# Performance work log

Measured on AMD Instinct MI355X. Metric: run time of the kernel, lower is better.

Reference implementation:

```python
import jax, jax.numpy as jnp
import numpy as np

D_MODEL = 768
NUM_HEADS = 12
D_K = D_MODEL // NUM_HEADS
B, T = 2, 4096


def setup_inputs() -> dict:
    key = jax.random.key(0)
    ks = jax.random.split(key, 5)
    x = jax.random.normal(ks[0], (B, T, D_MODEL), dtype=jnp.float32)
    # causal mask: True = masked (matches masked_fill semantics)
    mask = jnp.triu(jnp.ones((T, T), dtype=bool), k=1)
    W_qkv = jax.random.normal(ks[1], (D_MODEL, 3 * D_MODEL), dtype=jnp.float32) / np.sqrt(D_MODEL)
    b_qkv = jax.random.normal(ks[2], (3 * D_MODEL,), dtype=jnp.float32) * 0.02
    W_out = jax.random.normal(ks[3], (D_MODEL, D_MODEL), dtype=jnp.float32) / np.sqrt(D_MODEL)
    b_out = jax.random.normal(ks[4], (D_MODEL,), dtype=jnp.float32) * 0.02
    return {"x": x, "mask": mask, "W_qkv": W_qkv, "b_qkv": b_qkv, "W_out": W_out, "b_out": b_out}


def reference(x, mask, W_qkv, b_qkv, W_out, b_out):
    Bb, Tt, C = x.shape
    qkv = x @ W_qkv + b_qkv                       # [B,T,3C]
    # torch: reshape(B,T,H,3*d_k).transpose(1,2) then chunk on last dim
    qkv = qkv.reshape(Bb, Tt, NUM_HEADS, 3, D_K)  # split each head's 3*d_k chunk
    qkv = jnp.transpose(qkv, (0, 2, 1, 3, 4))     # [B,H,T,3,d_k]
    q, k, v = qkv[..., 0, :], qkv[..., 1, :], qkv[..., 2, :]
    scores = jnp.einsum('bhqd,bhkd->bhqk', q, k) / np.sqrt(D_K)
    scores = jnp.where(mask[None, None], -jnp.inf, scores)
    attn = jax.nn.softmax(scores, axis=-1)
    context = jnp.einsum('bhqk,bhkd->bhqd', attn, v)
    context = jnp.transpose(context, (0, 2, 1, 3)).reshape(Bb, Tt, C)
    return context @ W_out + b_out
```

## Files before the change

kernel.cpp:

```cpp
#include <hip/hip_runtime.h>
#include <hip/hip_bf16.h>
#include <stdint.h>


typedef __attribute__((ext_vector_type(8))) short bf16x8;
typedef __attribute__((ext_vector_type(4))) short bf16x4;
typedef __attribute__((ext_vector_type(4))) float f32x4;

#define TT 4096
#define NH 12
#define DK 64
#define DMODEL 768
#define NQKV 2304

__device__ __forceinline__ unsigned short f2bf(float f) {
    union { float f; unsigned u; } v; v.f = f;
    unsigned u = v.u;
    return (unsigned short)((u + 0x7fffu + ((u >> 16) & 1u)) >> 16);
}
__device__ __forceinline__ unsigned fbits(float f) {
    union { float f; unsigned u; } v; v.f = f; return v.u;
}
__device__ __forceinline__ unsigned pack_bf2(float a, float b) {
    return __builtin_amdgcn_perm(fbits(b) + 0x8000u, fbits(a) + 0x8000u, 0x07060302u);
}
__device__ __forceinline__ void glds16(const void* g, void* l) {
    __builtin_amdgcn_global_load_lds(
        (const __attribute__((address_space(1))) void*)g,
        (__attribute__((address_space(3))) void*)l, 16, 0, 0);
}

__global__ __launch_bounds__(256)
void prep(const float* __restrict__ x, unsigned short* __restrict__ xb,
          const float* __restrict__ Wq, unsigned short* __restrict__ Wqt,
          const float* __restrict__ Wo, unsigned short* __restrict__ Wot) {
    int b = blockIdx.x;
    if (b < 6144) {
        int i = (b * 256 + threadIdx.x) * 4;
        float4 v = *(const float4*)(x + i);
        uint2 u;
        u.x = pack_bf2(v.x, v.y);
        u.y = pack_bf2(v.z, v.w);
        *(uint2*)(xb + i) = u;
        return;
    }
    __shared__ unsigned short tile[64][65];
    const float* W; unsigned short* Wt; int K, N, bx, by;
    if (b < 6144 + 432) {
        int bb = b - 6144; bx = bb % 36; by = bb / 36;
        W = Wq; Wt = Wqt; K = DMODEL; N = NQKV;
    } else {
        int bb = b - 6576; bx = bb % 12; by = bb / 12;
        W = Wo; Wt = Wot; K = DMODEL; N = DMODEL;
    }
    int k0 = by * 64, n0 = bx * 64;
    int c = threadIdx.x & 63;
    int r0 = threadIdx.x >> 6;
    for (int p = 0; p < 16; ++p) {
        int r = r0 + p * 4;
        tile[r][c] = f2bf(W[(size_t)(k0 + r) * N + n0 + c]);
    }
    __syncthreads();
    for (int p = 0; p < 16; ++p) {
        int n = r0 + p * 4;
        Wt[(size_t)(n0 + n) * K + k0 + c] = tile[c][n];
    }
}

__global__ __launch_bounds__(256, 4)
void gemm_qkv(const unsigned short* __restrict__ Amat, const unsigned short* __restrict__ Bmat,
              const float* __restrict__ bias, unsigned short* __restrict__ qb,
              unsigned short* __restrict__ kb, unsigned short* __restrict__ vtb) {
    __shared__ unsigned short As[128 * 64];
    __shared__ unsigned short Bs[128 * 64];
    const int K = DMODEL;
    int bid = (int)blockIdx.y * 64 + (int)blockIdx.x;
    int idx = bid >> 3;
    int n0 = ((bid & 7) * 8 + (idx & 7)) * 128;
    int m0 = (idx >> 3) * 128;
    int tid = threadIdx.x, lane = tid & 63, w = tid >> 6;
    int wm = (w >> 1) * 64, wn = (w & 1) * 64;
    int quad = lane >> 4, lc = lane & 15;

    int gc8 = ((lane & 7) ^ (lane >> 3)) * 8;
    int row0 = w * 32 + (lane >> 3);
    const unsigned short* agp0 = Amat + (size_t)(m0 + row0) * K + gc8;
    const unsigned short* bgp0 = Bmat + (size_t)(n0 + row0) * K + gc8;
    unsigned short* alp0 = &As[w * 4 * 512];
    unsigned short* blp0 = &Bs[w * 4 * 512];

    int foff[2];
    for (int h = 0; h < 2; ++h)
        foff[h] = lc * 64 + (((quad + 4 * h) ^ (lc & 7)) * 8);

    f32x4 acc[4][4];
    for (int a = 0; a < 4; ++a)
        for (int b2 = 0; b2 < 4; ++b2) acc[a][b2] = (f32x4){0.f, 0.f, 0.f, 0.f};

    for (int k0 = 0; k0 < K; k0 += 64) {
        {
            const unsigned short* ag = agp0;
            const unsigned short* bg = bgp0;
            for (int p = 0; p < 4; ++p) {
                glds16(ag, alp0 + p * 512);
                glds16(bg, blp0 + p * 512);
                ag += 8 * DMODEL; bg += 8 * DMODEL;
            }
            agp0 += 64; bgp0 += 64;
        }
        __syncthreads();
        bf16x8 bfr[4][2];
        for (int nt = 0; nt < 4; ++nt)
            for (int h = 0; h < 2; ++h)
                bfr[nt][h] = *(const bf16x8*)(&Bs[wn * 64 + nt * 1024 + foff[h]]);
        for (int mt = 0; mt < 4; ++mt) {
            bf16x8 af0 = *(const bf16x8*)(&As[wm * 64 + mt * 1024 + foff[0]]);
            bf16x8 af1 = *(const bf16x8*)(&As[wm * 64 + mt * 1024 + foff[1]]);
            for (int nt = 0; nt < 4; ++nt) {
                acc[mt][nt] = __builtin_amdgcn_mfma_f32_16x16x32_bf16(
                    af0, bfr[nt][0], acc[mt][nt], 0, 0, 0);
                acc[mt][nt] = __builtin_amdgcn_mfma_f32_16x16x32_bf16(
                    af1, bfr[nt][1], acc[mt][nt], 0, 0, 0);
            }
        }
        __syncthreads();
    }
    const float c2q = 0.18033688f;
    for (int mt = 0; mt < 4; ++mt) {
        int colv = m0 + wm + mt * 16 + quad * 4;
        float4 bv = *(const float4*)(bias + colv);
        int h = colv / 192;
        int r = colv - h * 192;
        int which = r >> 6;
        int d0 = r & 63;
        for (int nt = 0; nt < 4; ++nt) {
            int tok = n0 + wn + nt * 16 + lc;
            int b = tok >> 12, t = tok & 4095;
            size_t bh = (size_t)(b * NH + h);
            float v0 = acc[mt][nt][0] + bv.x, v1 = acc[mt][nt][1] + bv.y;
            float v2 = acc[mt][nt][2] + bv.z, v3 = acc[mt][nt][3] + bv.w;
            if (which == 0) {
                uint2 u;
                u.x = pack_bf2(v0 * c2q, v1 * c2q);
                u.y = pack_bf2(v2 * c2q, v3 * c2q);
                *(uint2*)(qb + (bh * TT + t) * DK + d0) = u;
            } else if (which == 1) {
                uint2 u;
                u.x = pack_bf2(v0, v1);
                u.y = pack_bf2(v2, v3);
                *(uint2*)(kb + (bh * TT + t) * DK + d0) = u;
            } else {
                unsigned short* vp = vtb + (bh * DK + d0) * TT + t;
                vp[0] = f2bf(v0); vp[TT] = f2bf(v1);
                vp[2 * TT] = f2bf(v2); vp[3 * TT] = f2bf(v3);
            }
        }
    }
}

template <bool DIAG>
__device__ __forceinline__ void flash_tile(const unsigned short* __restrict__ Kb,
                                           const unsigned short* __restrict__ Vb,
                                           bf16x8 qf0, bf16x8 qf1,
                                           f32x4 (&o)[4], f32x4& ol,
                                           int kt, int q_lo, int quad, int lc) {
    int c0 = quad ^ (lc & 7);
    int sw = lc & 7;
    const bf16x4 ones = {(short)0x3F80, (short)0x3F80, (short)0x3F80, (short)0x3F80};
    for (int ktile = 0; ktile < 4; ++ktile) {
        bf16x8 kf0 = *(const bf16x8*)(&Kb[(ktile * 16 + lc) * 64 + c0 * 8]);
        bf16x8 kf1 = *(const bf16x8*)(&Kb[(ktile * 16 + lc) * 64 + (c0 ^ 4) * 8]);
        f32x4 s = (f32x4){0.f, 0.f, 0.f, 0.f};
        __builtin_amdgcn_s_setprio(1);
        s = __builtin_amdgcn_mfma_f32_16x16x32_bf16(kf0, qf0, s, 0, 0, 0);
        s = __builtin_amdgcn_mfma_f32_16x16x32_bf16(kf1, qf1, s, 0, 0, 0);
        __builtin_amdgcn_s_setprio(0);
        float p[4];
        if (DIAG) {
            int key0 = kt + ktile * 16 + quad * 4;
            int qcol = q_lo + lc;
            for (int i = 0; i < 4; ++i) {
                float e = __builtin_amdgcn_exp2f(s[i]);
                if (key0 + i > qcol) e = 0.f;
                p[i] = e;
            }
        } else {
            for (int i = 0; i < 4; ++i) p[i] = __builtin_amdgcn_exp2f(s[i]);
        }
        union { uint2 u; bf16x4 v; } pc;
        pc.u.x = pack_bf2(p[0], p[1]);
        pc.u.y = pack_bf2(p[2], p[3]);
        int c8 = (ktile * 2 + (quad >> 1)) ^ sw;
        int voff = c8 * 8 + (quad & 1) * 4;
        __builtin_amdgcn_s_setprio(1);
        ol = __builtin_amdgcn_mfma_f32_16x16x16bf16_1k(ones, pc.v, ol, 0, 0, 0);
        for (int dt = 0; dt < 4; ++dt) {
            bf16x4 vf = *(const bf16x4*)(&Vb[(dt * 16 + lc) * 64 + voff]);
            o[dt] = __builtin_amdgcn_mfma_f32_16x16x16bf16_1k(vf, pc.v, o[dt], 0, 0, 0);
        }
        __builtin_amdgcn_s_setprio(0);
    }
}

__global__ __launch_bounds__(256)
void flash_attn(const unsigned short* __restrict__ qbuf,
                const unsigned short* __restrict__ kbuf,
                const unsigned short* __restrict__ vtbuf,
                unsigned short* __restrict__ ctx) {
    __shared__ unsigned short Ks[2][64 * 64];
    __shared__ unsigned short Vs[2][64 * 64];
    int bh = blockIdx.x;
    int qblk = 63 - (int)blockIdx.y;
    int tid = threadIdx.x, lane = tid & 63, w = tid >> 6;
    int quad = lane >> 4, lc = lane & 15;
    const size_t base = (size_t)bh * TT * DK;
    int col8 = ((lane & 7) ^ (lane >> 3)) * 8;
    size_t hb = (size_t)(bh / NH) * TT * DMODEL + (size_t)(bh % NH) * DK;

    int q_lo = qblk * 64 + w * 16;
    int ntile = qblk + 1;

    int rb = (w & 1) * 4;
    const unsigned short* sgp[4];
    int stepEls;
    if (w < 2) {
        const unsigned short* kb0 = kbuf + base + (size_t)(lane >> 3) * DK + col8;
        for (int r = 0; r < 4; ++r) sgp[r] = kb0 + (size_t)((rb + r) * 8) * DK;
        stepEls = 64 * DK;
    } else {
        const unsigned short* vb0 = vtbuf + base + (size_t)(lane >> 3) * TT + col8;
        for (int r = 0; r < 4; ++r) sgp[r] = vb0 + (size_t)((rb + r) * 8) * TT;
        stepEls = 64;
    }

    bf16x8 qf0, qf1;
    {
        const unsigned short* qp = qbuf + base + (size_t)(q_lo + lc) * DK;
        qf0 = *(const bf16x8*)(qp + quad * 8);
        qf1 = *(const bf16x8*)(qp + 32 + quad * 8);
    }
    f32x4 o[4];
    for (int dt = 0; dt < 4; ++dt) o[dt] = (f32x4){0.f, 0.f, 0.f, 0.f};
    f32x4 ol = (f32x4){0.f, 0.f, 0.f, 0.f};

    {
        if (w < 2)
            for (int r = 0; r < 4; ++r) {
                glds16(sgp[r], &Ks[0][(rb + r) * 512]);
                sgp[r] += stepEls;
            }
        else
            for (int r = 0; r < 4; ++r) {
                glds16(sgp[r], &Vs[0][(rb + r) * 512]);
                sgp[r] += stepEls;
            }
    }
    __syncthreads();

    for (int ti = 0; ti < ntile; ++ti) {
        int cur = ti & 1;
        if (ti + 1 < ntile) {
            if (w < 2)
                for (int r = 0; r < 4; ++r) {
                    glds16(sgp[r], &Ks[cur ^ 1][(rb + r) * 512]);
                    sgp[r] += stepEls;
                }
            else
                for (int r = 0; r < 4; ++r) {
                    glds16(sgp[r], &Vs[cur ^ 1][(rb + r) * 512]);
                    sgp[r] += stepEls;
                }
        }
        int kt = ti * 64;
        if (ti == ntile - 1)
            flash_tile<true>(&Ks[cur][0], &Vs[cur][0], qf0, qf1, o, ol,
                             kt, q_lo, quad, lc);
        else
            flash_tile<false>(&Ks[cur][0], &Vs[cur][0], qf0, qf1, o, ol,
                              kt, q_lo, quad, lc);
        __syncthreads();
    }

    float inv = 1.f / ol[0];
    int t = q_lo + lc;
    unsigned short* cp = ctx + hb + (size_t)t * DMODEL;
    for (int dt = 0; dt < 4; ++dt) {
        uint2 u;
        u.x = pack_bf2(o[dt][0] * inv, o[dt][1] * inv);
        u.y = pack_bf2(o[dt][2] * inv, o[dt][3] * inv);
        *(uint2*)(cp + dt * 16 + quad * 4) = u;
    }
}

__global__ __launch_bounds__(256, 4)
void gemm_out(const unsigned short* __restrict__ Amat, const unsigned short* __restrict__ Bmat,
              const float* __restrict__ bias, float* __restrict__ out) {
    __shared__ unsigned short S[(64 + 128) * 64];
    const int K = DMODEL;
    int bid = (int)blockIdx.y * 64 + (int)blockIdx.x;
    int idx = bid >> 3;
    int n0 = ((bid & 7) * 8 + (idx & 7)) * 128;
    int m0 = (idx >> 3) * 64;
    int tid = threadIdx.x, lane = tid & 63, w = tid >> 6;
    int wm = (w & 1) * 32, wn = (w >> 1) * 64;
    int quad = lane >> 4, lc = lane & 15;

    const unsigned short* gp[6]; unsigned short* lp[6];
    for (int p = 0; p < 6; ++p) {
        int c = (w * 6 + p) * 64 + lane;
        if (c < 512) {
            int row = c >> 3, gc = (c & 7) ^ (row & 7);
            gp[p] = Amat + (size_t)(m0 + row) * K + gc * 8;
        } else {
            int cb = c - 512;
            int row = cb >> 3, gc = (cb & 7) ^ (row & 7);
            gp[p] = Bmat + (size_t)(n0 + row) * K + gc * 8;
        }
        lp[p] = &S[(w * 6 + p) * 512];
    }
    int foffA[2][2], foffB[4][2];
    for (int mt = 0; mt < 2; ++mt)
        for (int h = 0; h < 2; ++h)
            foffA[mt][h] = (wm + mt * 16 + lc) * 64 + (((quad + 4 * h) ^ (lc & 7)) * 8);
    for (int nt = 0; nt < 4; ++nt)
        for (int h = 0; h < 2; ++h)
            foffB[nt][h] = 4096 + (wn + nt * 16 + lc) * 64 + (((quad + 4 * h) ^ (lc & 7)) * 8);

    f32x4 acc[2][4];
    for (int a = 0; a < 2; ++a)
        for (int b2 = 0; b2 < 4; ++b2) acc[a][b2] = (f32x4){0.f, 0.f, 0.f, 0.f};

    for (int k0 = 0; k0 < K; k0 += 64) {
        for (int p = 0; p < 6; ++p) {
            glds16(gp[p], lp[p]);
            gp[p] += 64;
        }
        __syncthreads();
        bf16x8 af[2][2], bfr[4][2];
        for (int mt = 0; mt < 2; ++mt)
            for (int h = 0; h < 2; ++h) af[mt][h] = *(const bf16x8*)(&S[foffA[mt][h]]);
        for (int nt = 0; nt < 4; ++nt)
            for (int h = 0; h < 2; ++h) bfr[nt][h] = *(const bf16x8*)(&S[foffB[nt][h]]);
        for (int mt = 0; mt < 2; ++mt)
            for (int nt = 0; nt < 4; ++nt) {
                acc[mt][nt] = __builtin_amdgcn_mfma_f32_16x16x32_bf16(
                    af[mt][0], bfr[nt][0], acc[mt][nt], 0, 0, 0);
                acc[mt][nt] = __builtin_amdgcn_mfma_f32_16x16x32_bf16(
                    af[mt][1], bfr[nt][1], acc[mt][nt], 0, 0, 0);
            }
        __syncthreads();
    }
    for (int mt = 0; mt < 2; ++mt) {
        int colv = m0 + wm + mt * 16 + quad * 4;
        float4 bv = *(const float4*)(bias + colv);
        for (int nt = 0; nt < 4; ++nt) {
            int tok = n0 + wn + nt * 16 + lc;
            float4 ov;
            ov.x = acc[mt][nt][0] + bv.x;
            ov.y = acc[mt][nt][1] + bv.y;
            ov.z = acc[mt][nt][2] + bv.z;
            ov.w = acc[mt][nt][3] + bv.w;
            *(float4*)(out + (size_t)tok * DMODEL + colv) = ov;
        }
    }
}

extern "C" void kernel_launch(void* const* d_in, const int* in_sizes, int n_in,
                              void* d_out, int out_size, void* d_ws, size_t ws_size,
                              hipStream_t stream) {
    const float* x     = (const float*)d_in[0];
    const float* W_qkv = (const float*)d_in[2];
    const float* b_qkv = (const float*)d_in[3];
    const float* W_out = (const float*)d_in[4];
    const float* b_out = (const float*)d_in[5];
    float* out = (float*)d_out;

    unsigned short* ws = (unsigned short*)d_ws;
    unsigned short* Wqkv_t = ws;
    unsigned short* Wout_t = Wqkv_t + (size_t)NQKV * DMODEL;
    unsigned short* q_buf  = Wout_t + (size_t)DMODEL * DMODEL;
    unsigned short* k_buf  = q_buf  + (size_t)2 * NH * TT * DK;
    unsigned short* vt_buf = k_buf  + (size_t)2 * NH * TT * DK;
    unsigned short* ctx    = vt_buf + (size_t)2 * NH * TT * DK;
    unsigned short* x_bf   = ctx;

    prep<<<dim3(6720), 256, 0, stream>>>(x, x_bf, W_qkv, Wqkv_t, W_out, Wout_t);
    gemm_qkv<<<dim3((2 * TT) / 128, NQKV / 128), 256, 0, stream>>>(
        Wqkv_t, x_bf, b_qkv, q_buf, k_buf, vt_buf);
    flash_attn<<<dim3(2 * NH, TT / 64), 256, 0, stream>>>(q_buf, k_buf, vt_buf, ctx);
    gemm_out<<<dim3((2 * TT) / 128, DMODEL / 64), 256, 0, stream>>>(
        Wout_t, ctx, b_out, out);
}
```

Measured before the change: 254.8 us.

## Enlarge QKV GEMM M-tile to 192 and use hardware bf16 pack conversion

The QKV projection GEMM tile grows from 128x128 to 192x128 along the weight dimension, so each block does 6x4 MFMA sub-tiles per wave and the grid drops from 18 to 12 rows. Occupancy is lowered to 3 blocks per CU to make room for the larger accumulator set. Separately, the manual round-and-permute bf16 packing in the QKV epilogue, the attention P conversion and the context store is replaced with the native v_cvt_pk_bf16_f32 instruction. This cuts instruction count in the attention inner loop and raises operand reuse in the GEMM, at the cost of higher register pressure and fewer resident waves.

New measurement: 255.3 us (median of 2 runs). Within noise of the previous version (+0.2%).

```diff
diff --git a/kernel.cpp b/kernel.cpp
--- a/kernel.cpp
+++ b/kernel.cpp
@@ -23,6 +23,11 @@
 }
 __device__ __forceinline__ unsigned pack_bf2(float a, float b) {
     return __builtin_amdgcn_perm(fbits(b) + 0x8000u, fbits(a) + 0x8000u, 0x07060302u);
+}
+__device__ __forceinline__ unsigned cvt_pk_bf16(float a, float b) {
+    unsigned r;
+    asm("v_cvt_pk_bf16_f32 %0, %1, %2" : "=v"(r) : "v"(a), "v"(b));
+    return r;
 }
 __device__ __forceinline__ void glds16(const void* g, void* l) {
     __builtin_amdgcn_global_load_lds(
@@ -67,44 +72,48 @@
     }
 }
 
-__global__ __launch_bounds__(256, 4)
+__global__ __launch_bounds__(256, 3)
 void gemm_qkv(const unsigned short* __restrict__ Amat, const unsigned short* __restrict__ Bmat,
               const float* __restrict__ bias, unsigned short* __restrict__ qb,
               unsigned short* __restrict__ kb, unsigned short* __restrict__ vtb) {
-    __shared__ unsigned short As[128 * 64];
+    __shared__ unsigned short As[192 * 64];
     __shared__ unsigned short Bs[128 * 64];
     const int K = DMODEL;
     int bid = (int)blockIdx.y * 64 + (int)blockIdx.x;
     int idx = bid >> 3;
     int n0 = ((bid & 7) * 8 + (idx & 7)) * 128;
-    int m0 = (idx >> 3) * 128;
+    int m0 = (idx >> 3) * 192;
     int tid = threadIdx.x, lane = tid & 63, w = tid >> 6;
-    int wm = (w >> 1) * 64, wn = (w & 1) * 64;
+    int wm = (w >> 1) * 96, wn = (w & 1) * 64;
     int quad = lane >> 4, lc = lane & 15;
 
     int gc8 = ((lane & 7) ^ (lane >> 3)) * 8;
-    int row0 = w * 32 + (lane >> 3);
-    const unsigned short* agp0 = Amat + (size_t)(m0 + row0) * K + gc8;
-    const unsigned short* bgp0 = Bmat + (size_t)(n0 + row0) * K + gc8;
-    unsigned short* alp0 = &As[w * 4 * 512];
+    int arow0 = w * 48 + (lane >> 3);
+    int brow0 = w * 32 + (lane >> 3);
+    const unsigned short* agp0 = Amat + (size_t)(m0 + arow0) * K + gc8;
+    const unsigned short* bgp0 = Bmat + (size_t)(n0 + brow0) * K + gc8;
+    unsigned short* alp0 = &As[w * 6 * 512];
     unsigned short* blp0 = &Bs[w * 4 * 512];
 
     int foff[2];
     for (int h = 0; h < 2; ++h)
         foff[h] = lc * 64 + (((quad + 4 * h) ^ (lc & 7)) * 8);
 
-    f32x4 acc[4][4];
-    for (int a = 0; a < 4; ++a)
+    f32x4 acc[6][4];
+    for (int a = 0; a < 6; ++a)
         for (int b2 = 0; b2 < 4; ++b2) acc[a][b2] = (f32x4){0.f, 0.f, 0.f, 0.f};
 
     for (int k0 = 0; k0 < K; k0 += 64) {
         {
             const unsigned short* ag = agp0;
+            for (int p = 0; p < 6; ++p) {
+                glds16(ag, alp0 + p * 512);
+                ag += 8 * DMODEL;
+            }
             const unsigned short* bg = bgp0;
             for (int p = 0; p < 4; ++p) {
-                glds16(ag, alp0 + p * 512);
                 glds16(bg, blp0 + p * 512);
-                ag += 8 * DMODEL; bg += 8 * DMODEL;
+                bg += 8 * DMODEL;
             }
             agp0 += 64; bgp0 += 64;
         }
@@ -113,7 +122,7 @@
         for (int nt = 0; nt < 4; ++nt)
             for (int h = 0; h < 2; ++h)
                 bfr[nt][h] = *(const bf16x8*)(&Bs[wn * 64 + nt * 1024 + foff[h]]);
-        for (int mt = 0; mt < 4; ++mt) {
+        for (int mt = 0; mt < 6; ++mt) {
             bf16x8 af0 = *(const bf16x8*)(&As[wm * 64 + mt * 1024 + foff[0]]);
             bf16x8 af1 = *(const bf16x8*)(&As[wm * 64 + mt * 1024 + foff[1]]);
             for (int nt = 0; nt < 4; ++nt) {
@@ -126,7 +135,7 @@
         __syncthreads();
     }
     const float c2q = 0.18033688f;
-    for (int mt = 0; mt < 4; ++mt) {
+    for (int mt = 0; mt < 6; ++mt) {
         int colv = m0 + wm + mt * 16 + quad * 4;
         float4 bv = *(const float4*)(bias + colv);
         int h = colv / 192;
@@ -141,13 +150,13 @@
             float v2 = acc[mt][nt][2] + bv.z, v3 = acc[mt][nt][3] + bv.w;
             if (which == 0) {
                 uint2 u;
-                u.x = pack_bf2(v0 * c2q, v1 * c2q);
-                u.y = pack_bf2(v2 * c2q, v3 * c2q);
+                u.x = cvt_pk_bf16(v0 * c2q, v1 * c2q);
+                u.y = cvt_pk_bf16(v2 * c2q, v3 * c2q);
                 *(uint2*)(qb + (bh * TT + t) * DK + d0) = u;
             } else if (which == 1) {
                 uint2 u;
-                u.x = pack_bf2(v0, v1);
-                u.y = pack_bf2(v2, v3);
+                u.x = cvt_pk_bf16(v0, v1);
+                u.y = cvt_pk_bf16(v2, v3);
                 *(uint2*)(kb + (bh * TT + t) * DK + d0) = u;
             } else {
                 unsigned short* vp = vtb + (bh * DK + d0) * TT + t;
@@ -188,8 +197,8 @@
             for (int i = 0; i < 4; ++i) p[i] = __builtin_amdgcn_exp2f(s[i]);
         }
         union { uint2 u; bf16x4 v; } pc;
-        pc.u.x = pack_bf2(p[0], p[1]);
-        pc.u.y = pack_bf2(p[2], p[3]);
+        pc.u.x = cvt_pk_bf16(p[0], p[1]);
+        pc.u.y = cvt_pk_bf16(p[2], p[3]);
         int c8 = (ktile * 2 + (quad >> 1)) ^ sw;
         int voff = c8 * 8 + (quad & 1) * 4;
         __builtin_amdgcn_s_setprio(1);
@@ -286,8 +295,8 @@
     unsigned short* cp = ctx + hb + (size_t)t * DMODEL;
     for (int dt = 0; dt < 4; ++dt) {
         uint2 u;
-        u.x = pack_bf2(o[dt][0] * inv, o[dt][1] * inv);
-        u.y = pack_bf2(o[dt][2] * inv, o[dt][3] * inv);
+        u.x = cvt_pk_bf16(o[dt][0] * inv, o[dt][1] * inv);
+        u.y = cvt_pk_bf16(o[dt][2] * inv, o[dt][3] * inv);
         *(uint2*)(cp + dt * 16 + quad * 4) = u;
     }
 }
@@ -385,7 +394,7 @@
     unsigned short* x_bf   = ctx;
 
     prep<<<dim3(6720), 256, 0, stream>>>(x, x_bf, W_qkv, Wqkv_t, W_out, Wout_t);
-    gemm_qkv<<<dim3((2 * TT) / 128, NQKV / 128), 256, 0, stream>>>(
+    gemm_qkv<<<dim3((2 * TT) / 128, NQKV / 192), 256, 0, stream>>>(
         Wqkv_t, x_bf, b_qkv, q_buf, k_buf, vt_buf);
     flash_attn<<<dim3(2 * NH, TT / 64), 256, 0, stream>>>(q_buf, k_buf, vt_buf, ctx);
     gemm_out<<<dim3((2 * TT) / 128, DMODEL / 64), 256, 0, stream>>>(
```
